# Optimization experiments

Measured on AMD Instinct MI355X. Metric: run time of the kernel, lower is better.

The kernel has to match this reference:

```python
import jax, jax.numpy as jnp
import numpy as np

BLOCK = 32  # GGML Q8_0 block size: 32 int8 values share one scale


def setup_inputs() -> dict:
    key = jax.random.key(0)
    k1, k2, k3 = jax.random.split(key, 3)
    B, S, I, O = 2, 2048, 4096, 4096
    A = jax.random.normal(k1, (B, S, I), dtype=jnp.float32)
    # quantized weight values: stored unsigned 0..255, interpreted as signed (v - 128)
    w_q = jax.random.randint(k2, (O, I), 0, 255, dtype=jnp.int32)
    # one scale per block of 32 along infeatures
    scales = jax.random.uniform(k3, (O, I // BLOCK), dtype=jnp.float32) * 0.05
    return {"A": A, "w_q": w_q, "scales": scales}


def reference(A, w_q, scales):
    # Fused dequant + matmul (GGML Q8_0-style):
    # W[o, i] = (w_q[o, i] - 128) * scales[o, i // 32]
    O, I = w_q.shape
    q = w_q.astype(jnp.float32) - 128.0                      # [O, I]
    W = (q.reshape(O, I // BLOCK, BLOCK) * scales[:, :, None]).reshape(O, I)
    # C = A @ W^T, matching ggml mul_mat (weight is [outfeatures, infeatures])
    return jnp.einsum('bsi,oi->bso', A, W)
```

## Files before the change

kernel.cpp:

```cpp
#include <hip/hip_runtime.h>
#include <stdint.h>

typedef unsigned short u16;
typedef __bf16 bf16x8 __attribute__((ext_vector_type(8)));
typedef float f32x4 __attribute__((ext_vector_type(4)));
typedef unsigned short u16x8 __attribute__((ext_vector_type(8)));

__device__ __forceinline__ u16 f2bf(float f) {
  union { float f; uint32_t u; } x; x.f = f;
  uint32_t r = x.u + 0x7fffu + ((x.u >> 16) & 1u);
  return (u16)(r >> 16);
}

__global__ __launch_bounds__(256) void cvt_all(
    const float* __restrict__ A, u16* __restrict__ Ab, size_t n8a,
    const int* __restrict__ Wq, const float* __restrict__ S,
    u16* __restrict__ Wb, size_t n8w) {
  size_t i = (size_t)blockIdx.x * 256 + threadIdx.x;
  if (i < n8a) {
    const float4* p = (const float4*)(A + i * 8);
    float4 v0 = p[0], v1 = p[1];
    u16x8 r = { f2bf(v0.x), f2bf(v0.y), f2bf(v0.z), f2bf(v0.w),
                f2bf(v1.x), f2bf(v1.y), f2bf(v1.z), f2bf(v1.w) };
    *(u16x8*)(Ab + i * 8) = r;
  } else {
    size_t j = i - n8a;
    if (j >= n8w) return;
    const int4* p = (const int4*)(Wq + j * 8);
    int4 v0 = p[0], v1 = p[1];
    float s = S[j >> 2];
    u16x8 r = { f2bf((float)(v0.x - 128) * s), f2bf((float)(v0.y - 128) * s),
                f2bf((float)(v0.z - 128) * s), f2bf((float)(v0.w - 128) * s),
                f2bf((float)(v1.x - 128) * s), f2bf((float)(v1.y - 128) * s),
                f2bf((float)(v1.z - 128) * s), f2bf((float)(v1.w - 128) * s) };
    *(u16x8*)(Wb + j * 8) = r;
  }
}

#define BM 256
#define BN 128
#define BK 32

__device__ __forceinline__ void load_lds_16B(const void* g, void* l) {
  __builtin_amdgcn_global_load_lds(
      (const __attribute__((address_space(1))) unsigned int*)g,
      (__attribute__((address_space(3))) unsigned int*)l, 16, 0, 0);
}

template <int MODE>
__global__ __launch_bounds__(256, 2) void gemm_mode(
    const u16* __restrict__ Ab, const u16* __restrict__ Wb,
    const float* __restrict__ Af, const int* __restrict__ Wq,
    const float* __restrict__ Sc, float* __restrict__ C,
    int M, int N, int K) {
  __shared__ u16 As[BM * BK];
  __shared__ u16 Bs[BN * BK];

  const int tid = threadIdx.x;
  const int wave = tid >> 6, lane = tid & 63;
  const int m0 = blockIdx.y * BM, n0 = blockIdx.x * BN;
  const int wm = (wave & 1) * 128, wn = (wave >> 1) * 64;
  const int lrow = lane & 15, lq = lane >> 4;

  const u16* gA[4]; u16* dA[4];
  const u16* gB[2]; u16* dB[2];
  if constexpr (MODE == 0) {
    #pragma unroll
    for (int it = 0; it < 4; ++it) {
      int q = wave * 256 + it * 64 + lane;
      int row = q >> 2, s = q & 3;
      int c = (s - (row >> 1)) & 3;
      gA[it] = Ab + (size_t)(m0 + row) * K + c * 8;
      dA[it] = As + (size_t)(wave * 256 + it * 64) * 8;
    }
  }
  if constexpr (MODE <= 1) {
    #pragma unroll
    for (int it = 0; it < 2; ++it) {
      int q = wave * 128 + it * 64 + lane;
      int row = q >> 2, s = q & 3;
      int c = (s - (row >> 1)) & 3;
      gB[it] = Wb + (size_t)(n0 + row) * K + c * 8;
      dB[it] = Bs + (size_t)(wave * 128 + it * 64) * 8;
    }
  }

  const u16* fA[8]; const u16* fB[4];
  #pragma unroll
  for (int i = 0; i < 8; ++i) {
    int row = wm + i * 16 + lrow;
    int s = (lq + (row >> 1)) & 3;
    fA[i] = As + row * BK + s * 8;
  }
  #pragma unroll
  for (int j = 0; j < 4; ++j) {
    int row = wn + j * 16 + lrow;
    int s = (lq + (row >> 1)) & 3;
    fB[j] = Bs + row * BK + s * 8;
  }

  f32x4 acc[8][4] = {};

  for (int k0 = 0; k0 < K; k0 += BK) {
    if constexpr (MODE == 0) {
      #pragma unroll
      for (int it = 0; it < 4; ++it) load_lds_16B(gA[it] + k0, dA[it]);
      #pragma unroll
      for (int it = 0; it < 2; ++it) load_lds_16B(gB[it] + k0, dB[it]);
    } else {
      #pragma unroll
      for (int it = 0; it < 4; ++it) {
        int g = it * 256 + tid;
        int row = g >> 2, c8 = g & 3;
        int s = (c8 + (row >> 1)) & 3;
        const float4* p = (const float4*)(Af + (size_t)(m0 + row) * K + k0 + c8 * 8);
        float4 v0 = p[0], v1 = p[1];
        u16x8 r = { f2bf(v0.x), f2bf(v0.y), f2bf(v0.z), f2bf(v0.w),
                    f2bf(v1.x), f2bf(v1.y), f2bf(v1.z), f2bf(v1.w) };
        *(u16x8*)(As + row * BK + s * 8) = r;
      }
      if constexpr (MODE == 1) {
        #pragma unroll
        for (int it = 0; it < 2; ++it) load_lds_16B(gB[it] + k0, dB[it]);
      } else {
        #pragma unroll
        for (int it = 0; it < 2; ++it) {
          int g = it * 256 + tid;
          int row = g >> 2, c8 = g & 3;
          int s = (c8 + (row >> 1)) & 3;
          const int4* p = (const int4*)(Wq + (size_t)(n0 + row) * K + k0 + c8 * 8);
          int4 v0 = p[0], v1 = p[1];
          float sc = Sc[(size_t)(n0 + row) * (K >> 5) + (k0 >> 5)];
          u16x8 r = { f2bf((float)(v0.x - 128) * sc), f2bf((float)(v0.y - 128) * sc),
                      f2bf((float)(v0.z - 128) * sc), f2bf((float)(v0.w - 128) * sc),
                      f2bf((float)(v1.x - 128) * sc), f2bf((float)(v1.y - 128) * sc),
                      f2bf((float)(v1.z - 128) * sc), f2bf((float)(v1.w - 128) * sc) };
          *(u16x8*)(Bs + row * BK + s * 8) = r;
        }
      }
    }
    __syncthreads();

    bf16x8 a[8], b[4];
    #pragma unroll
    for (int i = 0; i < 8; ++i) a[i] = *(const bf16x8*)fA[i];
    #pragma unroll
    for (int j = 0; j < 4; ++j) b[j] = *(const bf16x8*)fB[j];
    #pragma unroll
    for (int i = 0; i < 8; ++i)
      #pragma unroll
      for (int j = 0; j < 4; ++j)
        acc[i][j] = __builtin_amdgcn_mfma_f32_16x16x32_bf16(a[i], b[j], acc[i][j], 0, 0, 0);
    __syncthreads();
  }

  #pragma unroll
  for (int i = 0; i < 8; ++i) {
    #pragma unroll
    for (int r = 0; r < 4; ++r) {
      int gm = m0 + wm + i * 16 + lq * 4 + r;
      float* crow = C + (size_t)gm * N + n0 + wn + lrow;
      #pragma unroll
      for (int j = 0; j < 4; ++j) crow[j * 16] = acc[i][j][r];
    }
  }
}

extern "C" void kernel_launch(void* const* d_in, const int* in_sizes, int n_in,
                              void* d_out, int out_size, void* d_ws, size_t ws_size,
                              hipStream_t stream) {
  const float* A  = (const float*)d_in[0];
  const int*   Wq = (const int*)d_in[1];
  const float* S  = (const float*)d_in[2];
  float* C = (float*)d_out;

  const int K = 4096;
  const int N = in_sizes[1] / K;
  const int M = in_sizes[0] / K;

  const size_t needA = (size_t)M * K * sizeof(u16);
  const size_t needW = (size_t)N * K * sizeof(u16);
  dim3 grid(N / BN, M / BM), blk(256);

  if (ws_size >= needA + needW) {
    u16* Ab = (u16*)d_ws;
    u16* Wb = (u16*)((char*)d_ws + needA);
    size_t nA8 = (size_t)M * K / 8, nW8 = (size_t)N * K / 8;
    cvt_all<<<(int)((nA8 + nW8 + 255) / 256), 256, 0, stream>>>(A, Ab, nA8, Wq, S, Wb, nW8);
    gemm_mode<0><<<grid, blk, 0, stream>>>(Ab, Wb, nullptr, nullptr, nullptr, C, M, N, K);
  } else if (ws_size >= needW) {
    u16* Wb = (u16*)d_ws;
    size_t nW8 = (size_t)N * K / 8;
    cvt_all<<<(int)((nW8 + 255) / 256), 256, 0, stream>>>(nullptr, nullptr, 0, Wq, S, Wb, nW8);
    gemm_mode<1><<<grid, blk, 0, stream>>>(nullptr, Wb, A, nullptr, nullptr, C, M, N, K);
  } else {
    gemm_mode<2><<<grid, blk, 0, stream>>>(nullptr, nullptr, A, Wq, S, C, M, N, K);
  }
}
```

Before: 303.5 us.

## Replace bf16 GEMM with 256x256x64 double-buffered 8-wave pipelined kernel

Adds a new main-path GEMM kernel with a 256x256 tile, BK=64, 512 threads and double-buffered LDS. It interleaves async global-to-LDS loads with MFMA quadrants under explicit barriers and vmcnt waits, XOR-swizzles the LDS layout, and remaps block IDs for L2 locality. The goal is to hide memory latency and raise data reuse per tile compared with the single-buffered 256x128x32 kernel. The cost is 128 KB of LDS per block, so occupancy may drop despite the launch bound of 2, and the hand-scheduled barriers are fragile.

```diff
diff --git a/kernel.cpp b/kernel.cpp
--- a/kernel.cpp
+++ b/kernel.cpp
@@ -37,43 +37,177 @@
   }
 }
 
-#define BM 256
-#define BN 128
-#define BK 32
-
 __device__ __forceinline__ void load_lds_16B(const void* g, void* l) {
   __builtin_amdgcn_global_load_lds(
       (const __attribute__((address_space(1))) unsigned int*)g,
       (__attribute__((address_space(3))) unsigned int*)l, 16, 0, 0);
 }
 
+#define BM 256
+#define BN 256
+#define BK 64
+
+#define BAR()   asm volatile("s_barrier" ::: "memory")
+#define VMBAR() asm volatile("s_waitcnt vmcnt(6)\n\ts_barrier" ::: "memory")
+
+__global__ __launch_bounds__(512, 2) void gemm8(
+    const u16* __restrict__ Ab, const u16* __restrict__ Wb,
+    float* __restrict__ C, int M, int N, int K) {
+  __shared__ u16 As[2][BM * BK];
+  __shared__ u16 Bs[2][BN * BK];
+
+  const int NT = K >> 6;
+  const int tid = (int)threadIdx.x;
+  const int wave = tid >> 6, lane = tid & 63;
+  const int wm = wave >> 2, wn = wave & 3;
+  const int lrow = lane & 15, lq = lane >> 4;
+
+  const int nbx = N / BN;
+  const int cpx = (int)gridDim.x >> 3;
+  const int swz = ((int)blockIdx.x & 7) * cpx + ((int)blockIdx.x >> 3);
+  const int m0 = (swz / nbx) * BM, n0 = (swz % nbx) * BN;
+
+  const int srow = lane >> 3, schunk = (lane & 7) ^ srow;
+  const u16* gA = Ab + (size_t)(m0 + srow) * K + schunk * 8;
+  const u16* gB = Wb + (size_t)(n0 + srow) * K + schunk * 8;
+  u16* const lA[2] = { &As[0][0], &As[1][0] };
+  u16* const lB[2] = { &Bs[0][0], &Bs[1][0] };
+
+  const int sx = lrow & 7;
+  const u16* baA[2][2]; const u16* baB[2][2];
+  #pragma unroll
+  for (int b = 0; b < 2; ++b)
+    #pragma unroll
+    for (int k2 = 0; k2 < 2; ++k2) {
+      baA[b][k2] = &As[b][(wm * 128 + lrow) * BK + (((k2 * 4 + lq) ^ sx) * 8)];
+      baB[b][k2] = &Bs[b][(wn * 64  + lrow) * BK + (((k2 * 4 + lq) ^ sx) * 8)];
+    }
+
+#define STAGE_A(BUF, MH, KT) do { if ((KT) < NT) { \
+    const size_t koff = (size_t)(KT) * BK; \
+    _Pragma("unroll") \
+    for (int it = 0; it < 2; ++it) { \
+      const int o = wave * 2 + it; \
+      const int rb = o * 8 + (o >> 3) * 64 + (MH) * 64; \
+      load_lds_16B(gA + (size_t)rb * K + koff, lA[BUF] + rb * BK); \
+    } } } while (0)
+
+#define STAGE_B(BUF, NH, KT) do { if ((KT) < NT) { \
+    const size_t koff = (size_t)(KT) * BK; \
+    _Pragma("unroll") \
+    for (int it = 0; it < 2; ++it) { \
+      const int o = wave * 2 + it; \
+      const int rb = (o >> 2) * 64 + (o & 3) * 8 + (NH) * 32; \
+      load_lds_16B(gB + (size_t)rb * K + koff, lB[BUF] + rb * BK); \
+    } } } while (0)
+
+#define LDA(DST, BUF, MH) do { \
+    _Pragma("unroll") \
+    for (int ii = 0; ii < 4; ++ii) \
+      _Pragma("unroll") \
+      for (int ks = 0; ks < 2; ++ks) \
+        DST[ii][ks] = *(const bf16x8*)(baA[BUF][ks] + ((MH) * 4 + ii) * 1024); \
+  } while (0)
+
+#define LDB(DST, BUF, NH) do { \
+    _Pragma("unroll") \
+    for (int jj = 0; jj < 2; ++jj) \
+      _Pragma("unroll") \
+      for (int ks = 0; ks < 2; ++ks) \
+        DST[jj][ks] = *(const bf16x8*)(baB[BUF][ks] + ((NH) * 2 + jj) * 1024); \
+  } while (0)
+
+#define QUAD(MH, NH, ASET, BSET) do { \
+    __builtin_amdgcn_s_setprio(1); \
+    _Pragma("unroll") \
+    for (int ii = 0; ii < 4; ++ii) \
+      _Pragma("unroll") \
+      for (int jj = 0; jj < 2; ++jj) { \
+        acc[(MH)*4+ii][(NH)*2+jj] = __builtin_amdgcn_mfma_f32_16x16x32_bf16( \
+            ASET[ii][0], BSET[jj][0], acc[(MH)*4+ii][(NH)*2+jj], 0, 0, 0); \
+        acc[(MH)*4+ii][(NH)*2+jj] = __builtin_amdgcn_mfma_f32_16x16x32_bf16( \
+            ASET[ii][1], BSET[jj][1], acc[(MH)*4+ii][(NH)*2+jj], 0, 0, 0); \
+      } \
+    __builtin_amdgcn_s_setprio(0); \
+  } while (0)
+
+  f32x4 acc[8][4] = {};
+  bf16x8 a0[4][2], a1[4][2], b0[2][2], b1[2][2];
+
+  STAGE_B(0, 0, 0); STAGE_A(0, 0, 0); STAGE_A(0, 1, 0); STAGE_B(0, 1, 0);
+  STAGE_B(1, 0, 1); STAGE_A(1, 0, 1); STAGE_A(1, 1, 1);
+  VMBAR();
+  LDA(a0, 0, 0); LDB(b0, 0, 0);
+
+#define HALF(T, BUF, NBUF) do { \
+     \
+    LDA(a1, BUF, 1); \
+    STAGE_B(NBUF, 1, (T) + 1); \
+    BAR(); \
+    QUAD(0, 0, a0, b0); \
+    BAR(); \
+     \
+    LDB(b1, BUF, 1); \
+    STAGE_B(BUF, 0, (T) + 2); \
+    BAR(); \
+    QUAD(1, 0, a1, b0); \
+    BAR(); \
+     \
+    STAGE_A(BUF, 0, (T) + 2); \
+    BAR(); \
+    QUAD(0, 1, a0, b1); \
+    BAR(); \
+     \
+    STAGE_A(BUF, 1, (T) + 2); \
+    VMBAR(); \
+    QUAD(1, 1, a1, b1); \
+    if ((T) + 1 < NT) { LDA(a0, NBUF, 0); LDB(b0, NBUF, 0); } \
+    BAR(); \
+  } while (0)
+
+  for (int t = 0; t < NT; t += 2) {
+    HALF(t, 0, 1);
+    HALF(t + 1, 1, 0);
+  }
+
+  #pragma unroll
+  for (int i = 0; i < 8; ++i)
+    #pragma unroll
+    for (int r = 0; r < 4; ++r) {
+      const int gm = m0 + wm * 128 + i * 16 + lq * 4 + r;
+      float* crow = C + (size_t)gm * N + n0 + wn * 64 + lrow;
+      #pragma unroll
+      for (int j = 0; j < 4; ++j) crow[j * 16] = acc[i][j][r];
+    }
+
+#undef HALF
+#undef QUAD
+#undef LDB
+#undef LDA
+#undef STAGE_B
+#undef STAGE_A
+}
+
+#define FBM 256
+#define FBN 128
+#define FBK 32
+
 template <int MODE>
-__global__ __launch_bounds__(256, 2) void gemm_mode(
+__global__ __launch_bounds__(256, 2) void gemm_fb(
     const u16* __restrict__ Ab, const u16* __restrict__ Wb,
     const float* __restrict__ Af, const int* __restrict__ Wq,
     const float* __restrict__ Sc, float* __restrict__ C,
     int M, int N, int K) {
-  __shared__ u16 As[BM * BK];
-  __shared__ u16 Bs[BN * BK];
+  __shared__ u16 As[FBM * FBK];
+  __shared__ u16 Bs[FBN * FBK];
 
   const int tid = threadIdx.x;
   const int wave = tid >> 6, lane = tid & 63;
-  const int m0 = blockIdx.y * BM, n0 = blockIdx.x * BN;
+  const int m0 = blockIdx.y * FBM, n0 = blockIdx.x * FBN;
   const int wm = (wave & 1) * 128, wn = (wave >> 1) * 64;
   const int lrow = lane & 15, lq = lane >> 4;
 
-  const u16* gA[4]; u16* dA[4];
   const u16* gB[2]; u16* dB[2];
-  if constexpr (MODE == 0) {
-    #pragma unroll
-    for (int it = 0; it < 4; ++it) {
-      int q = wave * 256 + it * 64 + lane;
-      int row = q >> 2, s = q & 3;
-      int c = (s - (row >> 1)) & 3;
-      gA[it] = Ab + (size_t)(m0 + row) * K + c * 8;
-      dA[it] = As + (size_t)(wave * 256 + it * 64) * 8;
-    }
-  }
   if constexpr (MODE <= 1) {
     #pragma unroll
     for (int it = 0; it < 2; ++it) {
@@ -90,53 +224,46 @@
   for (int i = 0; i < 8; ++i) {
     int row = wm + i * 16 + lrow;
     int s = (lq + (row >> 1)) & 3;
-    fA[i] = As + row * BK + s * 8;
+    fA[i] = As + row * FBK + s * 8;
   }
   #pragma unroll
   for (int j = 0; j < 4; ++j) {
     int row = wn + j * 16 + lrow;
     int s = (lq + (row >> 1)) & 3;
-    fB[j] = Bs + row * BK + s * 8;
+    fB[j] = Bs + row * FBK + s * 8;
   }
 
   f32x4 acc[8][4] = {};
 
-  for (int k0 = 0; k0 < K; k0 += BK) {
-    if constexpr (MODE == 0) {
-      #pragma unroll
-      for (int it = 0; it < 4; ++it) load_lds_16B(gA[it] + k0, dA[it]);
+  for (int k0 = 0; k0 < K; k0 += FBK) {
+    #pragma unroll
+    for (int it = 0; it < 4; ++it) {
+      int g = it * 256 + tid;
+      int row = g >> 2, c8 = g & 3;
+      int s = (c8 + (row >> 1)) & 3;
+      const float4* p = (const float4*)(Af + (size_t)(m0 + row) * K + k0 + c8 * 8);
+      float4 v0 = p[0], v1 = p[1];
+      u16x8 r = { f2bf(v0.x), f2bf(v0.y), f2bf(v0.z), f2bf(v0.w),
+                  f2bf(v1.x), f2bf(v1.y), f2bf(v1.z), f2bf(v1.w) };
+      *(u16x8*)(As + row * FBK + s * 8) = r;
+    }
+    if constexpr (MODE == 1) {
       #pragma unroll
       for (int it = 0; it < 2; ++it) load_lds_16B(gB[it] + k0, dB[it]);
     } else {
       #pragma unroll
-      for (int it = 0; it < 4; ++it) {
+      for (int it = 0; it < 2; ++it) {
         int g = it * 256 + tid;
         int row = g >> 2, c8 = g & 3;
         int s = (c8 + (row >> 1)) & 3;
-        const float4* p = (const float4*)(Af + (size_t)(m0 + row) * K + k0 + c8 * 8);
-        float4 v0 = p[0], v1 = p[1];
-        u16x8 r = { f2bf(v0.x), f2bf(v0.y), f2bf(v0.z), f2bf(v0.w),
-                    f2bf(v1.x), f2bf(v1.y), f2bf(v1.z), f2bf(v1.w) };
-        *(u16x8*)(As + row * BK + s * 8) = r;
-      }
-      if constexpr (MODE == 1) {
-        #pragma unroll
-        for (int it = 0; it < 2; ++it) load_lds_16B(gB[it] + k0, dB[it]);
-      } else {
-        #pragma unroll
-        for (int it = 0; it < 2; ++it) {
-          int g = it * 256 + tid;
-          int row = g >> 2, c8 = g & 3;
-          int s = (c8 + (row >> 1)) & 3;
-          const int4* p = (const int4*)(Wq + (size_t)(n0 + row) * K + k0 + c8 * 8);
-          int4 v0 = p[0], v1 = p[1];
-          float sc = Sc[(size_t)(n0 + row) * (K >> 5) + (k0 >> 5)];
-          u16x8 r = { f2bf((float)(v0.x - 128) * sc), f2bf((float)(v0.y - 128) * sc),
-                      f2bf((float)(v0.z - 128) * sc), f2bf((float)(v0.w - 128) * sc),
-                      f2bf((float)(v1.x - 128) * sc), f2bf((float)(v1.y - 128) * sc),
-                      f2bf((float)(v1.z - 128) * sc), f2bf((float)(v1.w - 128) * sc) };
-          *(u16x8*)(Bs + row * BK + s * 8) = r;
-        }
+        const int4* p = (const int4*)(Wq + (size_t)(n0 + row) * K + k0 + c8 * 8);
+        int4 v0 = p[0], v1 = p[1];
+        float sc = Sc[(size_t)(n0 + row) * (K >> 5) + (k0 >> 5)];
+        u16x8 r = { f2bf((float)(v0.x - 128) * sc), f2bf((float)(v0.y - 128) * sc),
+                    f2bf((float)(v0.z - 128) * sc), f2bf((float)(v0.w - 128) * sc),
+                    f2bf((float)(v1.x - 128) * sc), f2bf((float)(v1.y - 128) * sc),
+                    f2bf((float)(v1.z - 128) * sc), f2bf((float)(v1.w - 128) * sc) };
+        *(u16x8*)(Bs + row * FBK + s * 8) = r;
       }
     }
     __syncthreads();
@@ -180,20 +307,19 @@
 
   const size_t needA = (size_t)M * K * sizeof(u16);
   const size_t needW = (size_t)N * K * sizeof(u16);
-  dim3 grid(N / BN, M / BM), blk(256);
 
   if (ws_size >= needA + needW) {
     u16* Ab = (u16*)d_ws;
     u16* Wb = (u16*)((char*)d_ws + needA);
     size_t nA8 = (size_t)M * K / 8, nW8 = (size_t)N * K / 8;
     cvt_all<<<(int)((nA8 + nW8 + 255) / 256), 256, 0, stream>>>(A, Ab, nA8, Wq, S, Wb, nW8);
-    gemm_mode<0><<<grid, blk, 0, stream>>>(Ab, Wb, nullptr, nullptr, nullptr, C, M, N, K);
+    gemm8<<<dim3((M / BM) * (N / BN)), dim3(512), 0, stream>>>(Ab, Wb, C, M, N, K);
   } else if (ws_size >= needW) {
     u16* Wb = (u16*)d_ws;
     size_t nW8 = (size_t)N * K / 8;
     cvt_all<<<(int)((nW8 + 255) / 256), 256, 0, stream>>>(nullptr, nullptr, 0, Wq, S, Wb, nW8);
-    gemm_mode<1><<<grid, blk, 0, stream>>>(nullptr, Wb, A, nullptr, nullptr, C, M, N, K);
+    gemm_fb<1><<<dim3(N / FBN, M / FBM), dim3(256), 0, stream>>>(nullptr, Wb, A, nullptr, nullptr, C, M, N, K);
   } else {
-    gemm_mode<2><<<grid, blk, 0, stream>>>(nullptr, nullptr, A, Wq, S, C, M, N, K);
-  }
-}
+    gemm_fb<2><<<dim3(N / FBN, M / FBM), dim3(256), 0, stream>>>(nullptr, nullptr, A, Wq, S, C, M, N, K);
+  }
+}
```

New measurement: 418.5 us. 1.38x slower.
